# Kernel optimization log

Measured on AMD Instinct MI355X. Metric: run time of the kernel, lower is better.

## Reference

```python
import jax, jax.numpy as jnp
import numpy as np

EMBED_DIM = 1024
NUM_HEADS = 16
HEAD_DIM = EMBED_DIM // NUM_HEADS
B, T = 2, 2048


def setup_inputs() -> dict:
    key = jax.random.key(0)
    ks = jax.random.split(key, 9)
    s = 1.0 / np.sqrt(EMBED_DIM)
    return {
        "x": jax.random.normal(ks[0], (B, T, EMBED_DIM), dtype=jnp.float32),
        "W_q": jax.random.uniform(ks[1], (EMBED_DIM, EMBED_DIM), jnp.float32, -s, s),
        "b_q": jax.random.uniform(ks[2], (EMBED_DIM,), jnp.float32, -s, s),
        "W_k": jax.random.uniform(ks[3], (EMBED_DIM, EMBED_DIM), jnp.float32, -s, s),
        "b_k": jax.random.uniform(ks[4], (EMBED_DIM,), jnp.float32, -s, s),
        "W_v": jax.random.uniform(ks[5], (EMBED_DIM, EMBED_DIM), jnp.float32, -s, s),
        "b_v": jax.random.uniform(ks[6], (EMBED_DIM,), jnp.float32, -s, s),
        "W_o": jax.random.uniform(ks[7], (EMBED_DIM, EMBED_DIM), jnp.float32, -s, s),
        "b_o": jax.random.uniform(ks[8], (EMBED_DIM,), jnp.float32, -s, s),
    }


def reference(x, W_q, b_q, W_k, b_k, W_v, b_v, W_o, b_o):
    Bv, Tv, C = x.shape
    # QKV projections (torch Linear: x @ W.T + b); split into heads -> (B,H,T,Dh)
    def proj(W, b):
        return (x @ W.T + b).reshape(Bv, Tv, NUM_HEADS, HEAD_DIM).transpose(0, 2, 1, 3)
    q, k, v = proj(W_q, b_q), proj(W_k, b_k), proj(W_v, b_v)
    scale = 1.0 / np.sqrt(HEAD_DIM).astype(np.float32)
    scores = jnp.einsum("bhqd,bhkd->bhqk", q, k) * scale  # (B,H,T,T)
    causal = jnp.tril(jnp.ones((Tv, Tv), dtype=bool))
    scores = jnp.where(causal, scores, -jnp.inf)
    attn = jax.nn.softmax(scores, axis=-1)
    # dropout is identity in eval / p=0
    out = jnp.einsum("bhqk,bhkd->bhqd", attn, v)  # (B,H,T,Dh)
    out = out.transpose(0, 2, 1, 3).reshape(Bv, Tv, C)
    return out @ W_o.T + b_o
```

## Files before the change

kernel.cpp:

```cpp
#include <hip/hip_runtime.h>
#include <hip/hip_bf16.h>


typedef __bf16 bf16;
typedef __attribute__((ext_vector_type(8))) __bf16 bf16x8;
typedef __attribute__((ext_vector_type(4))) __bf16 bf16x4;
typedef __attribute__((ext_vector_type(4))) float floatx4;

#define LOG2E 1.44269504088896340736f

__device__ __forceinline__ void gl2lds16(const void* g, void* l) {
  __builtin_amdgcn_global_load_lds((const __attribute__((address_space(1))) void*)g,
                                   (__attribute__((address_space(3))) void*)l, 16, 0, 0);
}

__global__ __launch_bounds__(256) void cast_all(
    const float* __restrict__ x, const float* __restrict__ wq,
    const float* __restrict__ wk, const float* __restrict__ wv,
    const float* __restrict__ wo, bf16* __restrict__ dst)
{
  const size_t M1 = (size_t)1 << 20;
  size_t i4 = ((size_t)blockIdx.x * 256 + threadIdx.x) * 4;
  const float* src = x;
  size_t off = i4;
  if (i4 >= 4 * M1) {
    size_t r = i4 - 4 * M1;
    int seg = (int)(r >> 20);
    off = r & (M1 - 1);
    src = (seg == 0) ? wq : (seg == 1) ? wk : (seg == 2) ? wv : wo;
  }
  float4 f = *(const float4*)(src + off);
  bf16x4 o = { (bf16)f.x, (bf16)f.y, (bf16)f.z, (bf16)f.w };
  *(bf16x4*)(dst + i4) = o;
}

template<bool F32OUT, bool QKV, int BN>
__global__ __launch_bounds__(256, 2) void gemm_bt(
    const bf16* __restrict__ A, const bf16* __restrict__ Wb,
    const float* __restrict__ bq, const float* __restrict__ bk,
    const float* __restrict__ bv, void* __restrict__ outb,
    bf16* __restrict__ vt, int M, int N, int K, float qscale)
{
  __shared__ bf16 As[128 * 32];
  __shared__ bf16 Bs[BN * 32];
  const int tid = threadIdx.x;
  const int lane = tid & 63;
  const int wid = tid >> 6;
  const int l15 = lane & 15, l4 = lane >> 4;
  constexpr int I = (BN == 128) ? 4 : 2;
  const int wr = (BN == 128) ? (wid >> 1) : wid;
  const int wc = (BN == 128) ? (wid & 1) : 0;

  const bf16* W;
  const float* bias;
  float osc = 1.0f;
  int n0, mat = 0;
  bf16* outh;
  float* outf;
  if (QKV) {
    mat = blockIdx.x >> 3;
    n0 = (blockIdx.x & 7) << 7;
    W = Wb + ((size_t)mat << 20);
    bias = (mat == 0) ? bq : (mat == 1 ? bk : bv);
    if (mat == 0) osc = qscale;
    outh = (bf16*)outb + ((size_t)mat << 22);
    outf = nullptr;
  } else {
    n0 = blockIdx.x * BN;
    W = Wb;
    bias = bq;
    outf = (float*)outb;
    outh = nullptr;
  }
  const int m0 = blockIdx.y << 7;

  floatx4 acc[I][4] = {};

  for (int k0 = 0; k0 < K; k0 += 32) {
#pragma unroll
    for (int it = 0; it < 2; ++it) {
      int c = it * 256 + tid;
      int row = c >> 2, kof = (c & 3) << 3;
      gl2lds16(A + (size_t)(m0 + row) * K + k0 + kof, As + c * 8);
    }
#pragma unroll
    for (int it = 0; it < BN / 64; ++it) {
      int c = it * 256 + tid;
      int row = c >> 2, kof = (c & 3) << 3;
      gl2lds16(W + (size_t)(n0 + row) * K + k0 + kof, Bs + c * 8);
    }
    __syncthreads();
    bf16x8 af[I], bfr[4];
#pragma unroll
    for (int i = 0; i < I; ++i)
      af[i] = *(const bf16x8*)(As + (wr * (I * 16) + i * 16 + l15) * 32 + l4 * 8);
#pragma unroll
    for (int j = 0; j < 4; ++j)
      bfr[j] = *(const bf16x8*)(Bs + (wc * 64 + j * 16 + l15) * 32 + l4 * 8);
#pragma unroll
    for (int i = 0; i < I; ++i)
#pragma unroll
      for (int j = 0; j < 4; ++j)
        acc[i][j] = __builtin_amdgcn_mfma_f32_16x16x32_bf16(af[i], bfr[j], acc[i][j], 0, 0, 0);
    __syncthreads();
  }

  if (QKV && mat == 2) {
#pragma unroll
    for (int j = 0; j < 4; ++j) {
      int col = n0 + wc * 64 + j * 16 + l15;
      float bv_ = bias[col];
      int h = col >> 6, d = col & 63;
#pragma unroll
      for (int i = 0; i < I; ++i) {
        int row = m0 + wr * (I * 16) + i * 16 + l4 * 4;
        int bb = row >> 11, t = row & 2047;
        bf16x4 pk;
#pragma unroll
        for (int rg = 0; rg < 4; ++rg) pk[rg] = (bf16)(acc[i][j][rg] + bv_);
        *(bf16x4*)(vt + (((size_t)(bb * 16 + h)) << 17) + ((size_t)d << 11) + t) = pk;
      }
    }
    return;
  }

#pragma unroll
  for (int j = 0; j < 4; ++j) {
    int col = n0 + wc * 64 + j * 16 + l15;
    float bv_ = bias[col];
#pragma unroll
    for (int i = 0; i < I; ++i) {
#pragma unroll
      for (int rg = 0; rg < 4; ++rg) {
        int row = m0 + wr * (I * 16) + i * 16 + l4 * 4 + rg;
        float v = (acc[i][j][rg] + bv_) * osc;
        if (F32OUT) outf[(size_t)row * N + col] = v;
        else        outh[(size_t)row * N + col] = (bf16)v;
      }
    }
  }
}

__global__ __launch_bounds__(256, 3) void attn_kernel(
    const bf16* __restrict__ Q, const bf16* __restrict__ Kg,
    const bf16* __restrict__ Vt, bf16* __restrict__ AO)
{
  constexpr int T = 2048, C = 1024;
  __shared__ bf16 Ks[2][64 * 64];
  __shared__ bf16 Vts[2][64 * 64];
  __shared__ bf16 Ps[4][16 * 80];

  const int tid = threadIdx.x;
  const int lane = tid & 63;
  const int w = tid >> 6;
  const int l15 = lane & 15, l4 = lane >> 4;

  const int u = blockIdx.x;
  const int bh = u & 31;
  const int qt = 31 - (u >> 5);
  const int q0 = qt << 6;
  const size_t base = ((size_t)(bh >> 4) * T) * C + (bh & 15) * 64;
  const bf16* vtb = Vt + ((size_t)bh << 17);

  const int q = q0 + w * 16 + l15;

  bf16x8 qf[2];
  {
    const bf16* qp = Q + base + (size_t)q * C + l4 * 8;
    qf[0] = *(const bf16x8*)(qp);
    qf[1] = *(const bf16x8*)(qp + 32);
  }

  floatx4 o[4] = {};
  float mrow = -1e38f, lrow = 0.f;

  auto stageK = [&](int j0, int bufi) {
#pragma unroll
    for (int it = 0; it < 2; ++it) {
      int c = it * 256 + tid;
      int row = c >> 3, s = (c & 7) ^ (row & 7);
      gl2lds16(Kg + base + (size_t)(j0 + row) * C + s * 8, &Ks[bufi][c * 8]);
    }
  };
  auto stageV = [&](int j0, int bufi) {
#pragma unroll
    for (int it = 0; it < 2; ++it) {
      int c = it * 256 + tid;
      int row = c >> 3, s = (c & 7) ^ (row & 7);
      gl2lds16(vtb + ((size_t)row << 11) + j0 + s * 8, &Vts[bufi][c * 8]);
    }
  };

  const int nkt = qt + 1;
  stageK(0, 0);
  stageV(0, 0);

  for (int jt = 0; jt < nkt; ++jt) {
    __syncthreads();
    const int cur = jt & 1;
    if (jt + 1 < nkt) {
      stageK((jt + 1) << 6, cur ^ 1);
      stageV((jt + 1) << 6, cur ^ 1);
    }
    const int j0 = jt << 6;

    floatx4 s4[4] = {};
#pragma unroll
    for (int kk = 0; kk < 2; ++kk) {
      bf16x8 kf[4];
#pragma unroll
      for (int tj = 0; tj < 4; ++tj) {
        int r = tj * 16 + l15;
        int sl = (kk * 4 + l4) ^ (r & 7);
        kf[tj] = *(const bf16x8*)(&Ks[cur][r * 64 + sl * 8]);
      }
#pragma unroll
      for (int tj = 0; tj < 4; ++tj)
        s4[tj] = __builtin_amdgcn_mfma_f32_16x16x32_bf16(kf[tj], qf[kk], s4[tj], 0, 0, 0);
    }

    if (jt == nkt - 1) {
#pragma unroll
      for (int tj = 0; tj < 4; ++tj) {
        int j = j0 + tj * 16 + l4 * 4;
#pragma unroll
        for (int rg = 0; rg < 4; ++rg)
          if (j + rg > q) s4[tj][rg] = -3e38f;
      }
    }

    float mx = -3e38f;
#pragma unroll
    for (int tj = 0; tj < 4; ++tj)
#pragma unroll
      for (int rg = 0; rg < 4; ++rg)
        mx = fmaxf(mx, s4[tj][rg]);
    mx = fmaxf(mx, __shfl_xor(mx, 16, 64));
    mx = fmaxf(mx, __shfl_xor(mx, 32, 64));
    float mnew = fmaxf(mrow, mx);
    float al = __builtin_amdgcn_exp2f(mrow - mnew);
    mrow = mnew;
    float psum = 0.f;
#pragma unroll
    for (int tj = 0; tj < 4; ++tj)
#pragma unroll
      for (int rg = 0; rg < 4; ++rg) {
        float e = __builtin_amdgcn_exp2f(s4[tj][rg] - mnew);
        s4[tj][rg] = e;
        psum += e;
      }
    psum += __shfl_xor(psum, 16, 64);
    psum += __shfl_xor(psum, 32, 64);
    lrow = lrow * al + psum;

#pragma unroll
    for (int tj = 0; tj < 4; ++tj) {
      bf16x4 pk = { (bf16)s4[tj][0], (bf16)s4[tj][1],
                    (bf16)s4[tj][2], (bf16)s4[tj][3] };
      *(bf16x4*)(&Ps[w][l15 * 80 + tj * 16 + l4 * 4]) = pk;
    }

#pragma unroll
    for (int td = 0; td < 4; ++td)
#pragma unroll
      for (int rg = 0; rg < 4; ++rg)
        o[td][rg] *= al;

#pragma unroll
    for (int tk = 0; tk < 2; ++tk) {
      bf16x8 pf = *(const bf16x8*)(&Ps[w][l15 * 80 + tk * 32 + l4 * 8]);
#pragma unroll
      for (int td = 0; td < 4; ++td) {
        int r = td * 16 + l15;
        int sl = (tk * 4 + l4) ^ (r & 7);
        bf16x8 vf = *(const bf16x8*)(&Vts[cur][r * 64 + sl * 8]);
        o[td] = __builtin_amdgcn_mfma_f32_16x16x32_bf16(vf, pf, o[td], 0, 0, 0);
      }
    }
  }

  float inv = 1.0f / lrow;
#pragma unroll
  for (int td = 0; td < 4; ++td) {
    bf16x4 ok = { (bf16)(o[td][0] * inv), (bf16)(o[td][1] * inv),
                  (bf16)(o[td][2] * inv), (bf16)(o[td][3] * inv) };
    *(bf16x4*)(AO + base + (size_t)q * C + td * 16 + l4 * 4) = ok;
  }
}

extern "C" void kernel_launch(void* const* d_in, const int* in_sizes, int n_in,
                              void* d_out, int out_size, void* d_ws, size_t ws_size,
                              hipStream_t stream) {
  const float* x  = (const float*)d_in[0];
  const float* Wq = (const float*)d_in[1];
  const float* bq = (const float*)d_in[2];
  const float* Wk = (const float*)d_in[3];
  const float* bk = (const float*)d_in[4];
  const float* Wv = (const float*)d_in[5];
  const float* bv = (const float*)d_in[6];
  const float* Wo = (const float*)d_in[7];
  const float* bo = (const float*)d_in[8];

  bf16* ws = (bf16*)d_ws;
  const size_t M1 = (size_t)1 << 20;
  bf16* xb  = ws;
  bf16* wqb = ws + 4 * M1;
  bf16* wob = ws + 7 * M1;
  bf16* Qp  = ws + 8 * M1;
  bf16* Vtp = ws + 16 * M1;
  bf16* AOp = ws + 20 * M1;

  cast_all<<<8192, 256, 0, stream>>>(x, Wq, Wk, Wv, Wo, ws);
  gemm_bt<false, true, 128><<<dim3(24, 32), 256, 0, stream>>>(
      xb, wqb, bq, bk, bv, (void*)Qp, Vtp, 4096, 1024, 1024, 0.125f * LOG2E);
  attn_kernel<<<1024, 256, 0, stream>>>(Qp, Qp + 4 * M1, Vtp, AOp);
  gemm_bt<true, false, 64><<<dim3(16, 32), 256, 0, stream>>>(
      AOp, wob, bo, nullptr, nullptr, d_out, nullptr, 4096, 1024, 1024, 1.0f);
}
```

Measured before the change: 185.8 us.

## Widen GEMM K-tile with swizzled LDS and keep attention P in registers

The GEMM now stages 64-wide K tiles with an XOR-swizzled LDS layout, halving the loop iterations and barriers, and its occupancy hint rises to 3. The attention kernel drops the per-wave P staging buffer in LDS and feeds P straight from registers into 16x16x16 bf16 MFMAs, reading V as 4-element chunks. It also skips the O rescale when the row max is unchanged across the whole wave and raises its occupancy hint to 4. The trade-offs are twice as many MFMA instructions in the PV product, more LDS per GEMM block, and register pressure from the tighter launch bounds.

```diff
diff --git a/kernel.cpp b/kernel.cpp
--- a/kernel.cpp
+++ b/kernel.cpp
@@ -6,12 +6,27 @@
 typedef __attribute__((ext_vector_type(8))) __bf16 bf16x8;
 typedef __attribute__((ext_vector_type(4))) __bf16 bf16x4;
 typedef __attribute__((ext_vector_type(4))) float floatx4;
+typedef __attribute__((ext_vector_type(4))) short short4v;
 
 #define LOG2E 1.44269504088896340736f
 
 __device__ __forceinline__ void gl2lds16(const void* g, void* l) {
   __builtin_amdgcn_global_load_lds((const __attribute__((address_space(1))) void*)g,
                                    (__attribute__((address_space(3))) void*)l, 16, 0, 0);
+}
+
+__device__ __forceinline__ floatx4 mfma16(bf16x4 a, bf16x4 b, floatx4 c) {
+#if __has_builtin(__builtin_amdgcn_mfma_f32_16x16x16_bf16)
+  return __builtin_amdgcn_mfma_f32_16x16x16_bf16(a, b, c, 0, 0, 0);
+#elif __has_builtin(__builtin_amdgcn_mfma_f32_16x16x16bf16_1k)
+  return __builtin_amdgcn_mfma_f32_16x16x16bf16_1k(
+      __builtin_bit_cast(short4v, a), __builtin_bit_cast(short4v, b), c, 0, 0, 0);
+#else
+  floatx4 d = c;
+  asm volatile("v_mfma_f32_16x16x16_bf16 %0, %1, %2, %0"
+               : "+v"(d) : "v"(a), "v"(b));
+  return d;
+#endif
 }
 
 __global__ __launch_bounds__(256) void cast_all(
@@ -35,14 +50,14 @@
 }
 
 template<bool F32OUT, bool QKV, int BN>
-__global__ __launch_bounds__(256, 2) void gemm_bt(
+__global__ __launch_bounds__(256, 3) void gemm_bt(
     const bf16* __restrict__ A, const bf16* __restrict__ Wb,
     const float* __restrict__ bq, const float* __restrict__ bk,
     const float* __restrict__ bv, void* __restrict__ outb,
     bf16* __restrict__ vt, int M, int N, int K, float qscale)
 {
-  __shared__ bf16 As[128 * 32];
-  __shared__ bf16 Bs[BN * 32];
+  __shared__ bf16 As[128 * 64];
+  __shared__ bf16 Bs[BN * 64];
   const int tid = threadIdx.x;
   const int lane = tid & 63;
   const int wid = tid >> 6;
@@ -76,32 +91,41 @@
 
   floatx4 acc[I][4] = {};
 
-  for (int k0 = 0; k0 < K; k0 += 32) {
-#pragma unroll
-    for (int it = 0; it < 2; ++it) {
+  for (int k0 = 0; k0 < K; k0 += 64) {
+#pragma unroll
+    for (int it = 0; it < 4; ++it) {
       int c = it * 256 + tid;
-      int row = c >> 2, kof = (c & 3) << 3;
-      gl2lds16(A + (size_t)(m0 + row) * K + k0 + kof, As + c * 8);
-    }
-#pragma unroll
-    for (int it = 0; it < BN / 64; ++it) {
+      int row = c >> 3, gs = ((c & 7) ^ (row & 7)) << 3;
+      gl2lds16(A + (size_t)(m0 + row) * K + k0 + gs, As + c * 8);
+    }
+#pragma unroll
+    for (int it = 0; it < BN / 32; ++it) {
       int c = it * 256 + tid;
-      int row = c >> 2, kof = (c & 3) << 3;
-      gl2lds16(W + (size_t)(n0 + row) * K + k0 + kof, Bs + c * 8);
+      int row = c >> 3, gs = ((c & 7) ^ (row & 7)) << 3;
+      gl2lds16(W + (size_t)(n0 + row) * K + k0 + gs, Bs + c * 8);
     }
     __syncthreads();
-    bf16x8 af[I], bfr[4];
-#pragma unroll
-    for (int i = 0; i < I; ++i)
-      af[i] = *(const bf16x8*)(As + (wr * (I * 16) + i * 16 + l15) * 32 + l4 * 8);
-#pragma unroll
-    for (int j = 0; j < 4; ++j)
-      bfr[j] = *(const bf16x8*)(Bs + (wc * 64 + j * 16 + l15) * 32 + l4 * 8);
-#pragma unroll
-    for (int i = 0; i < I; ++i)
-#pragma unroll
-      for (int j = 0; j < 4; ++j)
-        acc[i][j] = __builtin_amdgcn_mfma_f32_16x16x32_bf16(af[i], bfr[j], acc[i][j], 0, 0, 0);
+#pragma unroll
+    for (int kk = 0; kk < 2; ++kk) {
+      bf16x8 af[I], bfr[4];
+#pragma unroll
+      for (int i = 0; i < I; ++i) {
+        int r = wr * (I * 16) + i * 16 + l15;
+        int g = (kk * 4 + l4) ^ (r & 7);
+        af[i] = *(const bf16x8*)(As + r * 64 + g * 8);
+      }
+#pragma unroll
+      for (int j = 0; j < 4; ++j) {
+        int r = wc * 64 + j * 16 + l15;
+        int g = (kk * 4 + l4) ^ (r & 7);
+        bfr[j] = *(const bf16x8*)(Bs + r * 64 + g * 8);
+      }
+#pragma unroll
+      for (int i = 0; i < I; ++i)
+#pragma unroll
+        for (int j = 0; j < 4; ++j)
+          acc[i][j] = __builtin_amdgcn_mfma_f32_16x16x32_bf16(af[i], bfr[j], acc[i][j], 0, 0, 0);
+    }
     __syncthreads();
   }
 
@@ -141,14 +165,13 @@
   }
 }
 
-__global__ __launch_bounds__(256, 3) void attn_kernel(
+__global__ __launch_bounds__(256, 4) void attn_kernel(
     const bf16* __restrict__ Q, const bf16* __restrict__ Kg,
     const bf16* __restrict__ Vt, bf16* __restrict__ AO)
 {
   constexpr int T = 2048, C = 1024;
   __shared__ bf16 Ks[2][64 * 64];
   __shared__ bf16 Vts[2][64 * 64];
-  __shared__ bf16 Ps[4][16 * 80];
 
   const int tid = threadIdx.x;
   const int lane = tid & 63;
@@ -159,8 +182,26 @@
   const int bh = u & 31;
   const int qt = 31 - (u >> 5);
   const int q0 = qt << 6;
+  const int nkt = qt + 1;
   const size_t base = ((size_t)(bh >> 4) * T) * C + (bh & 15) * 64;
   const bf16* vtb = Vt + ((size_t)bh << 17);
+
+  auto stageK = [&](int j0, int bufi) {
+#pragma unroll
+    for (int it = 0; it < 2; ++it) {
+      int c = it * 256 + tid;
+      int row = c >> 3, g = (c & 7) ^ (row & 7);
+      gl2lds16(Kg + base + (size_t)(j0 + row) * C + g * 8, &Ks[bufi][c * 8]);
+    }
+  };
+  auto stageV = [&](int j0, int bufi) {
+#pragma unroll
+    for (int it = 0; it < 2; ++it) {
+      int c = it * 256 + tid;
+      int d = c >> 3, g = (c & 7) ^ (d & 7);
+      gl2lds16(vtb + ((size_t)d << 11) + j0 + g * 8, &Vts[bufi][c * 8]);
+    }
+  };
 
   const int q = q0 + w * 16 + l15;
 
@@ -174,24 +215,6 @@
   floatx4 o[4] = {};
   float mrow = -1e38f, lrow = 0.f;
 
-  auto stageK = [&](int j0, int bufi) {
-#pragma unroll
-    for (int it = 0; it < 2; ++it) {
-      int c = it * 256 + tid;
-      int row = c >> 3, s = (c & 7) ^ (row & 7);
-      gl2lds16(Kg + base + (size_t)(j0 + row) * C + s * 8, &Ks[bufi][c * 8]);
-    }
-  };
-  auto stageV = [&](int j0, int bufi) {
-#pragma unroll
-    for (int it = 0; it < 2; ++it) {
-      int c = it * 256 + tid;
-      int row = c >> 3, s = (c & 7) ^ (row & 7);
-      gl2lds16(vtb + ((size_t)row << 11) + j0 + s * 8, &Vts[bufi][c * 8]);
-    }
-  };
-
-  const int nkt = qt + 1;
   stageK(0, 0);
   stageV(0, 0);
 
@@ -207,16 +230,13 @@
     floatx4 s4[4] = {};
 #pragma unroll
     for (int kk = 0; kk < 2; ++kk) {
-      bf16x8 kf[4];
 #pragma unroll
       for (int tj = 0; tj < 4; ++tj) {
         int r = tj * 16 + l15;
-        int sl = (kk * 4 + l4) ^ (r & 7);
-        kf[tj] = *(const bf16x8*)(&Ks[cur][r * 64 + sl * 8]);
-      }
-#pragma unroll
-      for (int tj = 0; tj < 4; ++tj)
-        s4[tj] = __builtin_amdgcn_mfma_f32_16x16x32_bf16(kf[tj], qf[kk], s4[tj], 0, 0, 0);
+        int g = (kk * 4 + l4) ^ (r & 7);
+        bf16x8 kf = *(const bf16x8*)(&Ks[cur][r * 64 + g * 8]);
+        s4[tj] = __builtin_amdgcn_mfma_f32_16x16x32_bf16(kf, qf[kk], s4[tj], 0, 0, 0);
+      }
     }
 
     if (jt == nkt - 1) {
@@ -240,41 +260,43 @@
     float mnew = fmaxf(mrow, mx);
     float al = __builtin_amdgcn_exp2f(mrow - mnew);
     mrow = mnew;
-    float psum = 0.f;
+    float ps = 0.f;
 #pragma unroll
     for (int tj = 0; tj < 4; ++tj)
 #pragma unroll
       for (int rg = 0; rg < 4; ++rg) {
         float e = __builtin_amdgcn_exp2f(s4[tj][rg] - mnew);
         s4[tj][rg] = e;
-        psum += e;
-      }
-    psum += __shfl_xor(psum, 16, 64);
-    psum += __shfl_xor(psum, 32, 64);
-    lrow = lrow * al + psum;
-
+        ps += e;
+      }
+    ps += __shfl_xor(ps, 16, 64);
+    ps += __shfl_xor(ps, 32, 64);
+    lrow = lrow * al + ps;
+
+    if (!__all(al == 1.f)) {
+#pragma unroll
+      for (int td = 0; td < 4; ++td)
+#pragma unroll
+        for (int rg = 0; rg < 4; ++rg)
+          o[td][rg] *= al;
+    }
+
+    bf16x4 pf[4];
 #pragma unroll
     for (int tj = 0; tj < 4; ++tj) {
       bf16x4 pk = { (bf16)s4[tj][0], (bf16)s4[tj][1],
                     (bf16)s4[tj][2], (bf16)s4[tj][3] };
-      *(bf16x4*)(&Ps[w][l15 * 80 + tj * 16 + l4 * 4]) = pk;
-    }
-
-#pragma unroll
-    for (int td = 0; td < 4; ++td)
-#pragma unroll
-      for (int rg = 0; rg < 4; ++rg)
-        o[td][rg] *= al;
-
-#pragma unroll
-    for (int tk = 0; tk < 2; ++tk) {
-      bf16x8 pf = *(const bf16x8*)(&Ps[w][l15 * 80 + tk * 32 + l4 * 8]);
+      pf[tj] = pk;
+    }
+
+#pragma unroll
+    for (int tj = 0; tj < 4; ++tj) {
 #pragma unroll
       for (int td = 0; td < 4; ++td) {
-        int r = td * 16 + l15;
-        int sl = (tk * 4 + l4) ^ (r & 7);
-        bf16x8 vf = *(const bf16x8*)(&Vts[cur][r * 64 + sl * 8]);
-        o[td] = __builtin_amdgcn_mfma_f32_16x16x32_bf16(vf, pf, o[td], 0, 0, 0);
+        int d = td * 16 + l15;
+        int g = (tj * 2 + (l4 >> 1)) ^ (d & 7);
+        bf16x4 vf = *(const bf16x4*)(&Vts[cur][d * 64 + g * 8 + (l4 & 1) * 4]);
+        o[td] = mfma16(vf, pf[tj], o[td]);
       }
     }
   }
```

New measurement: 180.0 us. 1.03x faster.
